# Kernel optimization log

Measured on AMD Instinct MI355X. Metric: run time of the kernel, lower is better.

The kernel has to match this reference:

```python
import jax, jax.numpy as jnp
import numpy as np

B, N, C = 4, 2048, 768
H, HD = 12, 64
RANK, ALPHA = 8, 16.0
SCALING = ALPHA / RANK
SCALE = HD ** -0.5


def setup_inputs() -> dict:
    key = jax.random.key(0)
    ks = jax.random.split(key, 10)
    return {
        "x": jax.random.normal(ks[0], (B, N, C), jnp.float32),
        "qkv_weight": jax.random.normal(ks[1], (3 * C, C), jnp.float32) * 0.02,
        "q_bias": jax.random.normal(ks[2], (C,), jnp.float32) * 0.02,
        "v_bias": jax.random.normal(ks[3], (C,), jnp.float32) * 0.02,
        "lora_A_qkv": jax.random.normal(ks[4], (RANK, C), jnp.float32) * 0.02,
        "lora_B_qkv": jax.random.normal(ks[5], (3 * C, RANK), jnp.float32) * 0.02,
        "proj_weight": jax.random.normal(ks[6], (C, C), jnp.float32) * 0.02,
        "proj_bias": jax.random.normal(ks[7], (C,), jnp.float32) * 0.02,
        "lora_A_proj": jax.random.normal(ks[8], (RANK, C), jnp.float32) * 0.02,
        "lora_B_proj": jax.random.normal(ks[9], (C, RANK), jnp.float32) * 0.02,
    }


def reference(x, qkv_weight, q_bias, v_bias, lora_A_qkv, lora_B_qkv,
              proj_weight, proj_bias, lora_A_proj, lora_B_proj):
    # qkv bias = [q_bias, zeros, v_bias]
    qkv_bias = jnp.concatenate([q_bias, jnp.zeros_like(v_bias), v_bias])
    qkv = jnp.einsum('bnc,oc->bno', x, qkv_weight) + qkv_bias  # [B,N,3C]
    # LoRA on qkv: (x @ A^T @ B^T) * scaling
    qkv = qkv + jnp.einsum('bnr,or->bno', jnp.einsum('bnc,rc->bnr', x, lora_A_qkv), lora_B_qkv) * SCALING
    qkv = qkv.reshape(B, N, 3, H, HD).transpose(2, 0, 3, 1, 4)  # [3,B,H,N,HD]
    q, k, v = qkv[0], qkv[1], qkv[2]
    attn = jnp.einsum('bhnd,bhmd->bhnm', q * SCALE, k)  # [B,H,N,N]
    attn = jax.nn.softmax(attn, axis=-1)
    out = jnp.einsum('bhnm,bhmd->bhnd', attn, v)
    out = out.transpose(0, 2, 1, 3).reshape(B, N, C)
    out = jnp.einsum('bnc,oc->bno', out, proj_weight) + proj_bias
    # NOTE: module applies proj LoRA to the OUTPUT of proj (faithful quirk)
    out = out + jnp.einsum('bnr,or->bno', jnp.einsum('bnc,rc->bnr', out, lora_A_proj), lora_B_proj) * SCALING
    return out
```

## Files before the change

### kernel.cpp

```cpp
#include <hip/hip_runtime.h>
#include <cstdint>
#include <cstddef>

typedef __bf16 bf16;
typedef __bf16 bf16x4_t __attribute__((ext_vector_type(4)));
typedef __bf16 bf16x8_t __attribute__((ext_vector_type(8)));
typedef float f32x4_t __attribute__((ext_vector_type(4)));
typedef unsigned int u32;
typedef u32 u32x2_t __attribute__((ext_vector_type(2)));

#define DEV __device__ __forceinline__

static constexpr int CD  = 768;
static constexpr int C3  = 2304;
static constexpr int SEQ = 2048;
static constexpr int NB  = 4;
static constexpr int NH  = 12;
static constexpr int HDM = 64;
static constexpr int BHN = NB * NH;
static constexpr float QSCALE = 0.125f * 1.44269504088896340736f;
static constexpr float DEFER_THR = 4.0f;

DEV void async16(const void* g, void* l) {
  __builtin_amdgcn_global_load_lds(
      (const __attribute__((address_space(1))) void*)g,
      (__attribute__((address_space(3))) void*)l, 16, 0, 0);
}

DEV int swz(int r) { return (r ^ (r >> 2)) & 3; }

DEV u32 pack_bf16(float lo, float hi) {
  unsigned short l = __builtin_bit_cast(unsigned short, (bf16)lo);
  unsigned short h = __builtin_bit_cast(unsigned short, (bf16)hi);
  return ((u32)h << 16) | (u32)l;
}

DEV float max3f(float a, float b, float c) { return fmaxf(fmaxf(a, b), c); }

__global__ void k_cast(const float* __restrict__ x, bf16* __restrict__ o, int n4) {
  int i = blockIdx.x * blockDim.x + threadIdx.x;
  int stride = gridDim.x * blockDim.x;
  for (; i < n4; i += stride) {
    float4 v = reinterpret_cast<const float4*>(x)[i];
    bf16x4_t b;
    b[0] = (bf16)v.x; b[1] = (bf16)v.y; b[2] = (bf16)v.z; b[3] = (bf16)v.w;
    reinterpret_cast<bf16x4_t*>(o)[i] = b;
  }
}

__global__ void k_prep_qkvw(const float* __restrict__ W, const float* __restrict__ Aq,
                            const float* __restrict__ Bq, bf16* __restrict__ We) {
  int idx = blockIdx.x * 256 + threadIdx.x;
  int o = idx / CD, c = idx % CD;
  float s = 0.f;
#pragma unroll
  for (int r = 0; r < 8; ++r) s += Bq[o * 8 + r] * Aq[r * CD + c];
  We[idx] = (bf16)(W[idx] + 2.0f * s);
}

__global__ void k_prep_T(const float* __restrict__ Ap, const float* __restrict__ Wp,
                         float* __restrict__ T) {
  __shared__ float part[4][64];
  const int r = blockIdx.x / 12, cp0 = (blockIdx.x % 12) * 64;
  const int kl = threadIdx.x >> 6, cpl = threadIdx.x & 63;
  float s = 0.f;
  const int c0 = kl * 192;
  for (int c = c0; c < c0 + 192; ++c)
    s += Ap[r * CD + c] * Wp[(size_t)c * CD + cp0 + cpl];
  part[kl][cpl] = s;
  __syncthreads();
  if (threadIdx.x < 64)
    T[r * CD + cp0 + threadIdx.x] = (part[0][threadIdx.x] + part[1][threadIdx.x]) +
                                    (part[2][threadIdx.x] + part[3][threadIdx.x]);
}

__global__ void k_prep_projw(const float* __restrict__ Wp, const float* __restrict__ Bp,
                             const float* __restrict__ T, bf16* __restrict__ We) {
  int idx = blockIdx.x * 256 + threadIdx.x;
  int o = idx / CD, cp = idx % CD;
  float s = 0.f;
#pragma unroll
  for (int r = 0; r < 8; ++r) s += Bp[o * 8 + r] * T[r * CD + cp];
  We[idx] = (bf16)(Wp[idx] + 2.0f * s);
}

__global__ void k_prep_beff(const float* __restrict__ bp, const float* __restrict__ Ap,
                            const float* __restrict__ Bp, float* __restrict__ be) {
  __shared__ float tl[8];
  const int tid = threadIdx.x;
  const int r = tid >> 5, cl = tid & 31;
  float part = 0.f;
  for (int c = cl; c < CD; c += 32) part += Ap[r * CD + c] * bp[c];
#pragma unroll
  for (int d = 1; d < 32; d <<= 1) part += __shfl_xor(part, d);
  if (cl == 0) tl[r] = part;
  __syncthreads();
  for (int o = tid; o < CD; o += 256) {
    float s = 0.f;
#pragma unroll
    for (int rr = 0; rr < 8; ++rr) s += Bp[o * 8 + rr] * tl[rr];
    be[o] = bp[o] + 2.0f * s;
  }
}

__global__ __launch_bounds__(512) void k_gemm0(
    const bf16* __restrict__ Ag, const bf16* __restrict__ Bg,
    const float* __restrict__ qb, const float* __restrict__ vb,
    bf16* __restrict__ Qo, bf16* __restrict__ Ko, bf16* __restrict__ Vt) {
  __shared__ bf16 lds[2][(256 + 128) * 32];
  const int tid = threadIdx.x;
  const int w = tid >> 6, lane = tid & 63;
  const int lr = lane & 15, lg = lane >> 4;
  const int m0 = blockIdx.y * 256, n0 = blockIdx.x * 128;
  const int wm = w >> 1, wn = w & 1;

  const int r0 = tid >> 2, gp0 = tid & 3;
  const bf16* gA0 = Ag + (size_t)(m0 + r0) * CD + (gp0 ^ swz(r0)) * 8;
  const bf16* gA1 = Ag + (size_t)(m0 + 128 + r0) * CD + (gp0 ^ swz(r0)) * 8;
  const bf16* gB0 = Bg + (size_t)(n0 + r0) * CD + (gp0 ^ swz(r0)) * 8;

  f32x4_t acc[4][4] = {};

  auto stage = [&](int buf, int kof) {
    char* base = (char*)&lds[buf][0];
    async16(gA0 + kof, base + w * 1024);
    async16(gA1 + kof, base + 8192 + w * 1024);
    async16(gB0 + kof, base + 16384 + w * 1024);
  };

  stage(0, 0);
  int cur = 0;
  const int NK = CD / 32;
  for (int kt = 0; kt < NK; ++kt) {
    __syncthreads();
    if (kt + 1 < NK) stage(cur ^ 1, (kt + 1) * 32);
    const char* ba = (const char*)&lds[cur][0];
    const char* bb = ba + 16384;
    bf16x8_t af[4], bfr[4];
#pragma unroll
    for (int mi = 0; mi < 4; ++mi) {
      int rr = wm * 64 + mi * 16 + lr;
      af[mi] = *(const bf16x8_t*)(ba + rr * 64 + ((lg ^ swz(rr)) * 16));
    }
#pragma unroll
    for (int ni = 0; ni < 4; ++ni) {
      int rr = wn * 64 + ni * 16 + lr;
      bfr[ni] = *(const bf16x8_t*)(bb + rr * 64 + ((lg ^ swz(rr)) * 16));
    }
#pragma unroll
    for (int mi = 0; mi < 4; ++mi)
#pragma unroll
      for (int ni = 0; ni < 4; ++ni)
        acc[mi][ni] = __builtin_amdgcn_mfma_f32_16x16x32_bf16(bfr[ni], af[mi], acc[mi][ni], 0, 0, 0);
    cur ^= 1;
  }

  const int t = n0 / CD;
  if (t != 2) {
#pragma unroll
    for (int mi = 0; mi < 4; ++mi) {
      const int m = m0 + wm * 64 + mi * 16 + lr;
      const int b = m >> 11, nn = m & 2047;
#pragma unroll
      for (int ni = 0; ni < 4; ++ni) {
        const int nb = n0 + wn * 64 + ni * 16 + lg * 4;
        const int rem = nb - t * CD;
        const int h = rem >> 6, hd = rem & 63;
        const size_t oa = ((size_t)((b * NH + h) * SEQ + nn)) * HDM + hd;
        bf16x4_t o4;
        if (t == 0) {
          const float4 bias = *(const float4*)(qb + rem);
          o4[0] = (bf16)((acc[mi][ni][0] + bias.x) * QSCALE);
          o4[1] = (bf16)((acc[mi][ni][1] + bias.y) * QSCALE);
          o4[2] = (bf16)((acc[mi][ni][2] + bias.z) * QSCALE);
          o4[3] = (bf16)((acc[mi][ni][3] + bias.w) * QSCALE);
          *(bf16x4_t*)(Qo + oa) = o4;
        } else {
#pragma unroll
          for (int j = 0; j < 4; ++j) o4[j] = (bf16)acc[mi][ni][j];
          *(bf16x4_t*)(Ko + oa) = o4;
        }
      }
    }
  } else {
    bf16* tl = (bf16*)&lds[0][0];
    const int h0 = (n0 - 2 * CD) >> 6;
    const int bq = m0 >> 11;
    const int mb = m0 & 2047;
    const int r2 = tid >> 2, c2 = (tid & 3) * 32;
#pragma unroll
    for (int half = 0; half < 2; ++half) {
      __syncthreads();
      if ((wm >> 1) == half) {
#pragma unroll
        for (int mi = 0; mi < 4; ++mi) {
          const int ml = (wm & 1) * 64 + mi * 16 + lr;
#pragma unroll
          for (int ni = 0; ni < 4; ++ni) {
            const int hd = ni * 16 + lg * 4;
            const int rem = (n0 - 2 * CD) + wn * 64 + hd;
            const float4 bias = *(const float4*)(vb + rem);
            bf16* row = tl + (wn * 64 + hd) * 136 + ml;
            row[0 * 136] = (bf16)(acc[mi][ni][0] + bias.x);
            row[1 * 136] = (bf16)(acc[mi][ni][1] + bias.y);
            row[2 * 136] = (bf16)(acc[mi][ni][2] + bias.z);
            row[3 * 136] = (bf16)(acc[mi][ni][3] + bias.w);
          }
        }
      }
      __syncthreads();
      bf16* dstv = Vt + ((size_t)((bq * NH + h0 + (r2 >> 6)) * HDM) + (r2 & 63)) * SEQ
                      + mb + half * 128 + c2;
      const bf16* srcv = tl + r2 * 136 + c2;
#pragma unroll
      for (int k2 = 0; k2 < 4; ++k2)
        *(bf16x8_t*)(dstv + k2 * 8) = *(const bf16x8_t*)(srcv + k2 * 8);
    }
  }
}

__global__ __launch_bounds__(256) void k_gemm1(
    const bf16* __restrict__ Ag, const bf16* __restrict__ Bg,
    const float* __restrict__ beff, float* __restrict__ Fo) {
  __shared__ bf16 lds[2][2][128 * 32];
  const int tid = threadIdx.x;
  const int w = tid >> 6, lane = tid & 63;
  const int lr = lane & 15, lg = lane >> 4;
  const int m0 = blockIdx.y * 128, n0 = blockIdx.x * 128;
  const int wm = w >> 1, wn = w & 1;

  const int r0 = tid >> 2, gp0 = tid & 3;
  const int r1 = 64 + r0;
  const bf16* gA0 = Ag + (size_t)(m0 + r0) * CD + (gp0 ^ swz(r0)) * 8;
  const bf16* gA1 = Ag + (size_t)(m0 + r1) * CD + (gp0 ^ swz(r1)) * 8;
  const bf16* gB0 = Bg + (size_t)(n0 + r0) * CD + (gp0 ^ swz(r0)) * 8;
  const bf16* gB1 = Bg + (size_t)(n0 + r1) * CD + (gp0 ^ swz(r1)) * 8;
  const int dd0 = w * 1024, dd1 = 4096 + w * 1024;

  f32x4_t acc[4][4] = {};

  auto stage = [&](int buf, int kof) {
    char* ba = (char*)&lds[buf][0][0];
    char* bb = (char*)&lds[buf][1][0];
    async16(gA0 + kof, ba + dd0);
    async16(gA1 + kof, ba + dd1);
    async16(gB0 + kof, bb + dd0);
    async16(gB1 + kof, bb + dd1);
  };

  stage(0, 0);
  int cur = 0;
  const int NK = CD / 32;
  for (int kt = 0; kt < NK; ++kt) {
    __syncthreads();
    if (kt + 1 < NK) stage(cur ^ 1, (kt + 1) * 32);
    const char* ba = (const char*)&lds[cur][0][0];
    const char* bb = (const char*)&lds[cur][1][0];
    bf16x8_t af[4], bfr[4];
#pragma unroll
    for (int mi = 0; mi < 4; ++mi) {
      int rr = wm * 64 + mi * 16 + lr;
      af[mi] = *(const bf16x8_t*)(ba + rr * 64 + ((lg ^ swz(rr)) * 16));
    }
#pragma unroll
    for (int ni = 0; ni < 4; ++ni) {
      int rr = wn * 64 + ni * 16 + lr;
      bfr[ni] = *(const bf16x8_t*)(bb + rr * 64 + ((lg ^ swz(rr)) * 16));
    }
#pragma unroll
    for (int mi = 0; mi < 4; ++mi)
#pragma unroll
      for (int ni = 0; ni < 4; ++ni)
        acc[mi][ni] = __builtin_amdgcn_mfma_f32_16x16x32_bf16(bfr[ni], af[mi], acc[mi][ni], 0, 0, 0);
    cur ^= 1;
  }

#pragma unroll
  for (int mi = 0; mi < 4; ++mi) {
    const int m = m0 + wm * 64 + mi * 16 + lr;
#pragma unroll
    for (int ni = 0; ni < 4; ++ni) {
      const int nb = n0 + wn * 64 + ni * 16 + lg * 4;
      const float4 be4 = *(const float4*)(beff + nb);
      float4 o;
      o.x = acc[mi][ni][0] + be4.x;
      o.y = acc[mi][ni][1] + be4.y;
      o.z = acc[mi][ni][2] + be4.z;
      o.w = acc[mi][ni][3] + be4.w;
      *(float4*)(Fo + (size_t)m * CD + nb) = o;
    }
  }
}

__global__ __launch_bounds__(256, 3) void k_attn(const bf16* __restrict__ Q,
                                                 const bf16* __restrict__ Kg,
                                                 const bf16* __restrict__ Vt,
                                                 bf16* __restrict__ Ao) {
  __shared__ bf16 Kl[2][64 * 64];
  __shared__ bf16 Vl[2][64 * 64];
  __shared__ bf16 P[4][32 * 72];
  const int tid = threadIdx.x;
  const int w = tid >> 6, lane = tid & 63;
  const int lq = lane & 15, lg = lane >> 4;
  const int L = blockIdx.x;
  const int qb = (L >> 3) & 15;
  const int bh = (L & 7) * 6 + (L >> 7);
  const int b = bh / NH, h = bh % NH;
  const int qrow0 = qb * 128 + w * 32;

  const bf16* Qp = Q + ((size_t)bh * SEQ + qrow0) * HDM;
  const bf16* Kp = Kg + (size_t)bh * SEQ * HDM;
  const bf16* Vp = Vt + (size_t)bh * HDM * SEQ;

  const int sr = tid >> 3, scs = tid & 7;
  const int sr2 = sr + 32;
  bf16* kb0 = &Kl[0][w * 512]; bf16* kb1 = &Kl[1][w * 512];
  bf16* vb0 = &Vl[0][w * 512]; bf16* vb1 = &Vl[1][w * 512];

  auto stageKV = [&](int buf, int kb) {
    bf16* kd = buf ? kb1 : kb0;
    bf16* vd = buf ? vb1 : vb0;
    async16(Kp + (size_t)(kb + sr) * HDM + ((scs ^ (sr & 7)) * 8), kd);
    async16(Kp + (size_t)(kb + sr2) * HDM + ((scs ^ (sr2 & 7)) * 8), kd + 2048);
    async16(Vp + (size_t)sr * SEQ + kb + ((scs ^ (sr & 7)) * 8), vd);
    async16(Vp + (size_t)sr2 * SEQ + kb + ((scs ^ (sr2 & 7)) * 8), vd + 2048);
  };

  bf16x8_t qf[2][2];
#pragma unroll
  for (int qh = 0; qh < 2; ++qh)
#pragma unroll
    for (int s = 0; s < 2; ++s)
      qf[qh][s] = *(const bf16x8_t*)(Qp + (size_t)(lq + 16 * qh) * HDM + s * 32 + lg * 8);

  bf16x8_t ones;
#pragma unroll
  for (int j = 0; j < 8; ++j) ones[j] = (bf16)1.0f;

  f32x4_t oacc[2][2][4] = {};
  float mrun[2][2] = {{-1e30f, -1e30f}, {-1e30f, -1e30f}};
  float lsum[2][2] = {{0.f, 0.f}, {0.f, 0.f}};
  bf16* Pl = &P[w][0];
  const int sw = lq & 7;

  stageKV(0, 0);
  int cur = 0;
  for (int kb = 0; kb < SEQ; kb += 64) {
    __syncthreads();
    if (kb + 64 < SEQ) stageKV(cur ^ 1, kb + 64);
    const bf16* Kc = &Kl[cur][0];
    const bf16* Vc = &Vl[cur][0];

    f32x4_t st[2][2][2];
#pragma unroll
    for (int c = 0; c < 2; ++c)
#pragma unroll
      for (int nt = 0; nt < 2; ++nt) {
        const int row = c * 32 + nt * 16 + lq;
        bf16x8_t k0 = *(const bf16x8_t*)(Kc + row * 64 + ((lg ^ sw) * 8));
        bf16x8_t k1 = *(const bf16x8_t*)(Kc + row * 64 + (((4 + lg) ^ sw) * 8));
#pragma unroll
        for (int qh = 0; qh < 2; ++qh) {
          f32x4_t z = {0.f, 0.f, 0.f, 0.f};
          z = __builtin_amdgcn_mfma_f32_16x16x32_bf16(k0, qf[qh][0], z, 0, 0, 0);
          st[c][nt][qh] = __builtin_amdgcn_mfma_f32_16x16x32_bf16(k1, qf[qh][1], z, 0, 0, 0);
        }
      }

#pragma unroll
    for (int c = 0; c < 2; ++c)
#pragma unroll
      for (int qh = 0; qh < 2; ++qh) {
        float m = max3f(st[c][0][qh][0], st[c][0][qh][1], st[c][0][qh][2]);
        float m2 = max3f(st[c][0][qh][3], st[c][1][qh][0], st[c][1][qh][1]);
        m = max3f(m, m2, st[c][1][qh][2]);
        m = fmaxf(m, st[c][1][qh][3]);
        m = fmaxf(m, __shfl_xor(m, 16));
        m = fmaxf(m, __shfl_xor(m, 32));
        if (__any(m > mrun[c][qh] + DEFER_THR)) {
          const float mnew = fmaxf(mrun[c][qh], m);
          const float corr = __builtin_amdgcn_exp2f(mrun[c][qh] - mnew);
          mrun[c][qh] = mnew;
          lsum[c][qh] *= corr;
#pragma unroll
          for (int dt = 0; dt < 4; ++dt)
#pragma unroll
            for (int j = 0; j < 4; ++j) oacc[c][qh][dt][j] *= corr;
        }
#pragma unroll
        for (int nt = 0; nt < 2; ++nt)
#pragma unroll
          for (int j = 0; j < 4; ++j)
            st[c][nt][qh][j] = __builtin_amdgcn_exp2f(st[c][nt][qh][j] - mrun[c][qh]);

#pragma unroll
        for (int nt = 0; nt < 2; ++nt) {
          u32x2_t pw = {pack_bf16(st[c][nt][qh][0], st[c][nt][qh][1]),
                        pack_bf16(st[c][nt][qh][2], st[c][nt][qh][3])};
          *(u32x2_t*)(Pl + (lq + 16 * qh) * 72 + c * 32 + nt * 16 + lg * 4) = pw;
        }
      }

#pragma unroll
    for (int c = 0; c < 2; ++c) {
      bf16x8_t pf[2];
#pragma unroll
      for (int qh = 0; qh < 2; ++qh) {
        pf[qh] = *(const bf16x8_t*)(Pl + (lq + 16 * qh) * 72 + c * 32 + lg * 8);
        const f32x4_t zz = {0.f, 0.f, 0.f, 0.f};
        f32x4_t srow = __builtin_amdgcn_mfma_f32_16x16x32_bf16(ones, pf[qh], zz, 0, 0, 0);
        lsum[c][qh] += srow[0];
      }
#pragma unroll
      for (int dt = 0; dt < 4; ++dt) {
        const int vrow = dt * 16 + lq;
        bf16x8_t vf = *(const bf16x8_t*)(Vc + vrow * 64 + (((c * 4 + lg) ^ sw) * 8));
#pragma unroll
        for (int qh = 0; qh < 2; ++qh)
          oacc[c][qh][dt] = __builtin_amdgcn_mfma_f32_16x16x32_bf16(vf, pf[qh], oacc[c][qh][dt], 0, 0, 0);
      }
    }
    cur ^= 1;
  }

#pragma unroll
  for (int qh = 0; qh < 2; ++qh) {
    const float mm = fmaxf(mrun[0][qh], mrun[1][qh]);
    const float c0 = __builtin_amdgcn_exp2f(mrun[0][qh] - mm);
    const float c1 = __builtin_amdgcn_exp2f(mrun[1][qh] - mm);
    const float inv = 1.0f / (lsum[0][qh] * c0 + lsum[1][qh] * c1);
    bf16* dst = Ao + ((size_t)b * SEQ + qrow0 + lq + 16 * qh) * CD + h * HDM;
#pragma unroll
    for (int dt = 0; dt < 4; ++dt) {
      bf16x4_t o4;
#pragma unroll
      for (int j = 0; j < 4; ++j)
        o4[j] = (bf16)((oacc[0][qh][dt][j] * c0 + oacc[1][qh][dt][j] * c1) * inv);
      *(bf16x4_t*)(dst + dt * 16 + lg * 4) = o4;
    }
  }
}

extern "C" void kernel_launch(void* const* d_in, const int* in_sizes, int n_in,
                              void* d_out, int out_size, void* d_ws, size_t ws_size,
                              hipStream_t stream) {
  const float* x    = (const float*)d_in[0];
  const float* qkvw = (const float*)d_in[1];
  const float* qb   = (const float*)d_in[2];
  const float* vb   = (const float*)d_in[3];
  const float* Aq   = (const float*)d_in[4];
  const float* Bq   = (const float*)d_in[5];
  const float* Wp   = (const float*)d_in[6];
  const float* bp   = (const float*)d_in[7];
  const float* Ap   = (const float*)d_in[8];
  const float* Bp   = (const float*)d_in[9];
  float* out = (float*)d_out;

  char* ws = (char*)d_ws;
  size_t off = 0;
  auto alloc = [&](size_t bytes) {
    void* p = ws + off;
    off += (bytes + 511) & ~size_t(511);
    return p;
  };
  const size_t M = (size_t)NB * SEQ;
  bf16* xb   = (bf16*)alloc(M * CD * 2);
  bf16* Wqe  = (bf16*)alloc((size_t)C3 * CD * 2);
  bf16* Wpe  = (bf16*)alloc((size_t)CD * CD * 2);
  float* T   = (float*)alloc(8 * CD * 4);
  float* be  = (float*)alloc(CD * 4);
  bf16* Qb   = (bf16*)alloc((size_t)BHN * SEQ * HDM * 2);
  bf16* Kb   = (bf16*)alloc((size_t)BHN * SEQ * HDM * 2);
  bf16* Vtb  = (bf16*)alloc((size_t)BHN * SEQ * HDM * 2);
  bf16* attn = xb;

  k_cast<<<2048, 256, 0, stream>>>(x, xb, (int)(M * CD / 4));
  k_prep_qkvw<<<(C3 * CD) / 256, 256, 0, stream>>>(qkvw, Aq, Bq, Wqe);
  k_prep_T<<<96, 256, 0, stream>>>(Ap, Wp, T);
  k_prep_projw<<<(CD * CD) / 256, 256, 0, stream>>>(Wp, Bp, T, Wpe);
  k_prep_beff<<<1, 256, 0, stream>>>(bp, Ap, Bp, be);

  k_gemm0<<<dim3(C3 / 128, M / 256), 512, 0, stream>>>(
      xb, Wqe, qb, vb, Qb, Kb, Vtb);
  k_attn<<<(SEQ / 128) * BHN, 256, 0, stream>>>(Qb, Kb, Vtb, attn);
  k_gemm1<<<dim3(CD / 128, M / 128), 256, 0, stream>>>(attn, Wpe, be, out);
}
```

Before: 203.2 us.

## Merge prep kernels, remap GEMM blocks per XCD, unroll attention double-buffer loop

Folds the cast, qkv weight merge, T and bias prep kernels into one launch that dispatches on block index, cutting launch count and gaps between kernels. Both GEMMs switch to a 1D grid with a block remapping that groups consecutive M tiles onto the same XCD (L&7), aiming for better L2 reuse. The attention K/V loop is manually unrolled by two so the buffer index is a compile-time constant. pack_bf16 is rewritten using a bf16x2 vector bitcast.

```diff
diff --git a/kernel.cpp b/kernel.cpp
--- a/kernel.cpp
+++ b/kernel.cpp
@@ -3,6 +3,7 @@
 #include <cstddef>
 
 typedef __bf16 bf16;
+typedef __bf16 bf16x2_t __attribute__((ext_vector_type(2)));
 typedef __bf16 bf16x4_t __attribute__((ext_vector_type(4)));
 typedef __bf16 bf16x8_t __attribute__((ext_vector_type(8)));
 typedef float f32x4_t __attribute__((ext_vector_type(4)));
@@ -30,48 +31,69 @@
 DEV int swz(int r) { return (r ^ (r >> 2)) & 3; }
 
 DEV u32 pack_bf16(float lo, float hi) {
-  unsigned short l = __builtin_bit_cast(unsigned short, (bf16)lo);
-  unsigned short h = __builtin_bit_cast(unsigned short, (bf16)hi);
-  return ((u32)h << 16) | (u32)l;
+  bf16x2_t v;
+  v[0] = (bf16)lo;
+  v[1] = (bf16)hi;
+  return __builtin_bit_cast(u32, v);
 }
 
 DEV float max3f(float a, float b, float c) { return fmaxf(fmaxf(a, b), c); }
 
-__global__ void k_cast(const float* __restrict__ x, bf16* __restrict__ o, int n4) {
-  int i = blockIdx.x * blockDim.x + threadIdx.x;
-  int stride = gridDim.x * blockDim.x;
-  for (; i < n4; i += stride) {
-    float4 v = reinterpret_cast<const float4*>(x)[i];
-    bf16x4_t b;
-    b[0] = (bf16)v.x; b[1] = (bf16)v.y; b[2] = (bf16)v.z; b[3] = (bf16)v.w;
-    reinterpret_cast<bf16x4_t*>(o)[i] = b;
-  }
-}
-
-__global__ void k_prep_qkvw(const float* __restrict__ W, const float* __restrict__ Aq,
-                            const float* __restrict__ Bq, bf16* __restrict__ We) {
-  int idx = blockIdx.x * 256 + threadIdx.x;
-  int o = idx / CD, c = idx % CD;
-  float s = 0.f;
-#pragma unroll
-  for (int r = 0; r < 8; ++r) s += Bq[o * 8 + r] * Aq[r * CD + c];
-  We[idx] = (bf16)(W[idx] + 2.0f * s);
-}
-
-__global__ void k_prep_T(const float* __restrict__ Ap, const float* __restrict__ Wp,
-                         float* __restrict__ T) {
-  __shared__ float part[4][64];
-  const int r = blockIdx.x / 12, cp0 = (blockIdx.x % 12) * 64;
-  const int kl = threadIdx.x >> 6, cpl = threadIdx.x & 63;
-  float s = 0.f;
-  const int c0 = kl * 192;
-  for (int c = c0; c < c0 + 192; ++c)
-    s += Ap[r * CD + c] * Wp[(size_t)c * CD + cp0 + cpl];
-  part[kl][cpl] = s;
-  __syncthreads();
-  if (threadIdx.x < 64)
-    T[r * CD + cp0 + threadIdx.x] = (part[0][threadIdx.x] + part[1][threadIdx.x]) +
-                                    (part[2][threadIdx.x] + part[3][threadIdx.x]);
+__global__ void k_prep_a(const float* __restrict__ x, bf16* __restrict__ xb,
+                         const float* __restrict__ W, const float* __restrict__ Aq,
+                         const float* __restrict__ Bq, bf16* __restrict__ We,
+                         const float* __restrict__ Ap, const float* __restrict__ Wp,
+                         float* __restrict__ T,
+                         const float* __restrict__ bp, const float* __restrict__ Bp,
+                         float* __restrict__ be) {
+  __shared__ float smem[4][64];
+  const int bid = blockIdx.x, tid = threadIdx.x;
+  if (bid < 6912) {
+    int idx = bid * 256 + tid;
+    int o = idx / CD, c = idx % CD;
+    float s = 0.f;
+#pragma unroll
+    for (int r = 0; r < 8; ++r) s += Bq[o * 8 + r] * Aq[r * CD + c];
+    We[idx] = (bf16)(W[idx] + 2.0f * s);
+  } else if (bid < 7008) {
+    const int lb = bid - 6912;
+    const int r = lb / 12, cp0 = (lb % 12) * 64;
+    const int kl = tid >> 6, cpl = tid & 63;
+    float s = 0.f;
+    const int c0 = kl * 192;
+    for (int c = c0; c < c0 + 192; ++c)
+      s += Ap[r * CD + c] * Wp[(size_t)c * CD + cp0 + cpl];
+    smem[kl][cpl] = s;
+    __syncthreads();
+    if (tid < 64)
+      T[r * CD + cp0 + tid] = (smem[0][tid] + smem[1][tid]) +
+                              (smem[2][tid] + smem[3][tid]);
+  } else if (bid == 7008) {
+    float* tl = &smem[0][0];
+    const int r = tid >> 5, cl = tid & 31;
+    float part = 0.f;
+    for (int c = cl; c < CD; c += 32) part += Ap[r * CD + c] * bp[c];
+#pragma unroll
+    for (int d = 1; d < 32; d <<= 1) part += __shfl_xor(part, d);
+    if (cl == 0) tl[r] = part;
+    __syncthreads();
+    for (int o = tid; o < CD; o += 256) {
+      float s = 0.f;
+#pragma unroll
+      for (int rr = 0; rr < 8; ++rr) s += Bp[o * 8 + rr] * tl[rr];
+      be[o] = bp[o] + 2.0f * s;
+    }
+  } else {
+    const int n4 = (int)((size_t)NB * SEQ * CD / 4);
+    int i = (bid - 7009) * 256 + tid;
+    const int stride = 2048 * 256;
+    for (; i < n4; i += stride) {
+      float4 v = reinterpret_cast<const float4*>(x)[i];
+      bf16x4_t b;
+      b[0] = (bf16)v.x; b[1] = (bf16)v.y; b[2] = (bf16)v.z; b[3] = (bf16)v.w;
+      reinterpret_cast<bf16x4_t*>(xb)[i] = b;
+    }
+  }
 }
 
 __global__ void k_prep_projw(const float* __restrict__ Wp, const float* __restrict__ Bp,
@@ -82,25 +104,6 @@
 #pragma unroll
   for (int r = 0; r < 8; ++r) s += Bp[o * 8 + r] * T[r * CD + cp];
   We[idx] = (bf16)(Wp[idx] + 2.0f * s);
-}
-
-__global__ void k_prep_beff(const float* __restrict__ bp, const float* __restrict__ Ap,
-                            const float* __restrict__ Bp, float* __restrict__ be) {
-  __shared__ float tl[8];
-  const int tid = threadIdx.x;
-  const int r = tid >> 5, cl = tid & 31;
-  float part = 0.f;
-  for (int c = cl; c < CD; c += 32) part += Ap[r * CD + c] * bp[c];
-#pragma unroll
-  for (int d = 1; d < 32; d <<= 1) part += __shfl_xor(part, d);
-  if (cl == 0) tl[r] = part;
-  __syncthreads();
-  for (int o = tid; o < CD; o += 256) {
-    float s = 0.f;
-#pragma unroll
-    for (int rr = 0; rr < 8; ++rr) s += Bp[o * 8 + rr] * tl[rr];
-    be[o] = bp[o] + 2.0f * s;
-  }
 }
 
 __global__ __launch_bounds__(512) void k_gemm0(
@@ -111,7 +114,10 @@
   const int tid = threadIdx.x;
   const int w = tid >> 6, lane = tid & 63;
   const int lr = lane & 15, lg = lane >> 4;
-  const int m0 = blockIdx.y * 256, n0 = blockIdx.x * 128;
+  const int L = blockIdx.x;
+  const int idx = L >> 3;
+  const int m0 = ((L & 7) * 4 + idx / 18) * 256;
+  const int n0 = (idx % 18) * 128;
   const int wm = w >> 1, wn = w & 1;
 
   const int r0 = tid >> 2, gp0 = tid & 3;
@@ -226,7 +232,10 @@
   const int tid = threadIdx.x;
   const int w = tid >> 6, lane = tid & 63;
   const int lr = lane & 15, lg = lane >> 4;
-  const int m0 = blockIdx.y * 128, n0 = blockIdx.x * 128;
+  const int L = blockIdx.x;
+  const int idx = L >> 3;
+  const int m0 = ((L & 7) * 8 + idx / 6) * 128;
+  const int n0 = (idx % 6) * 128;
   const int wm = w >> 1, wn = w & 1;
 
   const int r0 = tid >> 2, gp0 = tid & 3;
@@ -343,13 +352,11 @@
   bf16* Pl = &P[w][0];
   const int sw = lq & 7;
 
-  stageKV(0, 0);
-  int cur = 0;
-  for (int kb = 0; kb < SEQ; kb += 64) {
+  auto body = [&](const int curbuf, const int kb) {
     __syncthreads();
-    if (kb + 64 < SEQ) stageKV(cur ^ 1, kb + 64);
-    const bf16* Kc = &Kl[cur][0];
-    const bf16* Vc = &Vl[cur][0];
+    if (kb + 64 < SEQ) stageKV(curbuf ^ 1, kb + 64);
+    const bf16* Kc = &Kl[curbuf][0];
+    const bf16* Vc = &Vl[curbuf][0];
 
     f32x4_t st[2][2][2];
 #pragma unroll
@@ -420,7 +427,12 @@
           oacc[c][qh][dt] = __builtin_amdgcn_mfma_f32_16x16x32_bf16(vf, pf[qh], oacc[c][qh][dt], 0, 0, 0);
       }
     }
-    cur ^= 1;
+  };
+
+  stageKV(0, 0);
+  for (int kb = 0; kb < SEQ; kb += 128) {
+    body(0, kb);
+    body(1, kb + 64);
   }
 
 #pragma unroll
@@ -474,14 +486,10 @@
   bf16* Vtb  = (bf16*)alloc((size_t)BHN * SEQ * HDM * 2);
   bf16* attn = xb;
 
-  k_cast<<<2048, 256, 0, stream>>>(x, xb, (int)(M * CD / 4));
-  k_prep_qkvw<<<(C3 * CD) / 256, 256, 0, stream>>>(qkvw, Aq, Bq, Wqe);
-  k_prep_T<<<96, 256, 0, stream>>>(Ap, Wp, T);
+  k_prep_a<<<9057, 256, 0, stream>>>(x, xb, qkvw, Aq, Bq, Wqe, Ap, Wp, T, bp, Bp, be);
   k_prep_projw<<<(CD * CD) / 256, 256, 0, stream>>>(Wp, Bp, T, Wpe);
-  k_prep_beff<<<1, 256, 0, stream>>>(bp, Ap, Bp, be);
-
-  k_gemm0<<<dim3(C3 / 128, M / 256), 512, 0, stream>>>(
-      xb, Wqe, qb, vb, Qb, Kb, Vtb);
+
+  k_gemm0<<<576, 512, 0, stream>>>(xb, Wqe, qb, vb, Qb, Kb, Vtb);
   k_attn<<<(SEQ / 128) * BHN, 256, 0, stream>>>(Qb, Kb, Vtb, attn);
-  k_gemm1<<<dim3(CD / 128, M / 128), 256, 0, stream>>>(attn, Wpe, be, out);
-}
+  k_gemm1<<<384, 256, 0, stream>>>(attn, Wpe, be, out);
+}
```

Measured after the change: 180.7 us. 11.1% less time.
